# Kernel optimization log

Measured on AMD Instinct MI355X. Metric: run time of the kernel, lower is better.

Reference implementation:

```python
import jax, jax.numpy as jnp
import numpy as np

IN_DIM = 3
OUT_DIM = 3
HSI_DIM = 31
MIN_BAND = 400.0
MAX_BAND = 700.0
N_BAND = 31  # == HSI_DIM so the indexed write fills every column
BN_EPS = 1e-5


def setup_inputs() -> dict:
    key = jax.random.key(0)
    ks = jax.random.split(key, 8)
    B, H, W = 16, 256, 256
    x = jax.random.uniform(ks[0], (B, H, W, IN_DIM), jnp.float32)
    x_hsi = jax.random.uniform(ks[1], (B, H, W, HSI_DIM), jnp.float32)
    conv_w = jax.random.normal(ks[2], (64, IN_DIM, 3, 3), jnp.float32) * 0.1
    conv_b = jax.random.normal(ks[3], (64,), jnp.float32) * 0.1
    bn_w = 1.0 + jax.random.normal(ks[4], (64,), jnp.float32) * 0.1
    bn_b = jax.random.normal(ks[5], (64,), jnp.float32) * 0.1
    fc_w = jax.random.normal(ks[6], (OUT_DIM + 2, 64), jnp.float32) * 0.1
    fc_b = jax.random.normal(ks[7], (OUT_DIM + 2,), jnp.float32) * 0.1
    return {"x": x, "x_hsi": x_hsi, "conv_w": conv_w, "conv_b": conv_b,
            "bn_w": bn_w, "bn_b": bn_b, "fc_w": fc_w, "fc_b": fc_b}


def _voltage_net(x, conv_w, conv_b, bn_w, bn_b, fc_w, fc_b):
    # x: (B, H, W, 3) channels-last -> NCHW
    xp = jnp.transpose(x, (0, 3, 1, 2))
    y = jax.lax.conv_general_dilated(
        xp, conv_w, window_strides=(1, 1), padding='SAME',
        dimension_numbers=('NCHW', 'OIHW', 'NCHW')) + conv_b[None, :, None, None]
    # BatchNorm2d (training-mode batch statistics, biased variance)
    mu = y.mean(axis=(0, 2, 3))
    var = y.var(axis=(0, 2, 3))
    y = (y - mu[None, :, None, None]) * jax.lax.rsqrt(var + BN_EPS)[None, :, None, None]
    y = y * bn_w[None, :, None, None] + bn_b[None, :, None, None]
    y = jax.nn.relu(y)
    feat = y.mean(axis=(2, 3))                      # AdaptiveAvgPool2d(1) -> (B, 64)
    raw = feat @ fc_w.T + fc_b                      # (B, out_dim + 2)
    mn = raw.min(axis=1, keepdims=True)
    mx = raw.max(axis=1, keepdims=True)
    norm = (raw - mn) / (mx - mn + 1e-8)
    mid = jnp.sort(norm, axis=1)[:, 1:-1]           # drop smallest & largest
    return mid * 10.0                               # (B, out_dim) voltages


def reference(x, x_hsi, conv_w, conv_b, bn_w, bn_b, fc_w, fc_b):
    voltages = _voltage_net(x, conv_w, conv_b, bn_w, bn_b, fc_w, fc_b)  # (B, C)
    # Vectorized Lyot SRF (replaces per-batch python loop); nBand == hsi_dim
    n = jnp.arange(N_BAND, dtype=jnp.float32)
    band = MIN_BAND + (MAX_BAND - MIN_BAND) * n / N_BAND                # (A,)
    cos_part = jnp.cos(2.0 * jnp.pi * (-0.01) / voltages)               # (B, C)
    srf = (0.5 - 0.5 * cos_part)[:, :, None] / (band[None, None, :] * 1e-6)  # (B, C, A)
    # contract hyperspectral bands: (B,C,A) x (B,H,W,A) -> (B,H,W,C)
    return jnp.einsum('bca,bpqa->bpqc', srf, x_hsi)
```

## Files before the change

kernel.cpp:

```cpp
#include <hip/hip_runtime.h>
#include <hip/hip_bf16.h>
#include <math.h>

#define BB 16
#define HH 256
#define WW 256

#define OFF_CHSUM 0
#define OFF_CHSQ  64
#define OFF_FEAT  256
#define OFF_Z     2048

#define SM_PAN   0
#define SM_W     21728
#define SM_B     28640
#define SM_RED   28896
#define SM_G     31744
#define SM_BYTES 32000

typedef __attribute__((ext_vector_type(8))) short bf16x8;
typedef __attribute__((ext_vector_type(4))) float f32x4;

union BFu { __hip_bfloat16 h; short s; };
union ABu { bf16x8 v; unsigned u[4]; };

__device__ __forceinline__ unsigned packsplit(float v) {
    BFu hi; hi.h = __float2bfloat16(v);
    float rs = v - __bfloat162float(hi.h);
    BFu lo; lo.h = __float2bfloat16(rs);
    return (unsigned)(unsigned short)hi.s | ((unsigned)(unsigned short)lo.s << 16);
}

__global__ void k_init(float* __restrict__ ws) {
    int i = blockIdx.x * 256 + threadIdx.x;
    if (i < 1280) ws[i] = 0.f;
}

template <int MODE>
__global__ __launch_bounds__(256) void k_convz(const float* __restrict__ x,
                                               const float* __restrict__ xh,
                                               const float* __restrict__ cw,
                                               const float* __restrict__ cb,
                                               const float* __restrict__ bnw,
                                               const float* __restrict__ bnb,
                                               float* __restrict__ ws) {
    __shared__ __align__(16) char smem[SM_BYTES];
    const int t = threadIdx.x;
    const int b = blockIdx.y;

    if (blockIdx.x >= 64) {
        float* s_x = (float*)smem;
        float* s_g = (float*)(smem + SM_G);
        const int zx = blockIdx.x - 64;
        if (t < 31) {
            const float band = 400.f + (300.f * (float)t) / 31.f;
            s_g[t] = 1.f / (band * 1e-6f);
        }
#pragma unroll 1
        for (int c = 0; c < 8; ++c) {
            const size_t pxbase = (size_t)b * 65536 + zx * 2048 + c * 256;
            const float4* xg = (const float4*)(xh + pxbase * 31);
            float4* sx4 = (float4*)s_x;
#pragma unroll
            for (int i = 0; i < 8; ++i) {
                int idx = t + (i << 8);
                if (idx < 1984) sx4[idx] = xg[idx];
            }
            __syncthreads();
            float z = 0.f;
            const float* px = s_x + t * 31;
#pragma unroll
            for (int a = 0; a < 31; ++a) z = fmaf(px[a], s_g[a], z);
            ws[OFF_Z + pxbase + t] = z;
            __syncthreads();
        }
        return;
    }

    unsigned* pan32 = (unsigned*)smem;
    float* s_w = (float*)(smem + SM_W);
    float* s_b = (float*)(smem + SM_B);
    float (*red)[4][16][2] = (float (*)[4][16][2])(smem + SM_RED);

    const int lane = t & 63;
    const int wv   = t >> 6;
    const int r0   = blockIdx.x * 4;
    const int mrow = lane & 15;
    const int s    = lane >> 4;
    const bool s3  = (s == 3);
    const float* __restrict__ xb = x + (size_t)b * (HH * WW * 3);

    for (int i = t; i < 1728; i += 256) s_w[i] = cw[i];
    if (t < 64) s_b[t] = cb[t];

    for (int e = t; e < 6 * 774; e += 256) {
        const int l = e / 774, j = e - l * 774;
        const int gr = r0 - 1 + l, gcf = j - 3;
        const bool ok = ((unsigned)gr < 256u) && ((unsigned)gcf < 768u);
        int off = gr * 768 + gcf;
        off = ok ? off : 0;
        float v = xb[off];
        v = ok ? v : 0.f;
        pan32[l * 776 + j] = packsplit(v);
    }
    for (int j = t; j < 776; j += 256) pan32[6 * 776 + j] = 0x3F80u;

    float av[4], bvv[4];
#pragma unroll
    for (int n = 0; n < 4; ++n) {
        const int ch = n * 16 + mrow;
        if (MODE == 1) {
            const float invN = 1.f / 1048576.f;
            const float mu = ws[OFF_CHSUM + ch] * invN;
            const float vr = ws[OFF_CHSQ + ch] * invN - mu * mu;
            const float rs = rsqrtf(vr + 1e-5f);
            av[n]  = rs * bnw[ch];
            bvv[n] = bnb[ch] - mu * av[n];
        } else { av[n] = 1.f; bvv[n] = 0.f; }
    }

    int off8[8];
#pragma unroll
    for (int e = 0; e < 8; ++e) {
        if (!s3)        off8[e] = (wv + s) * 776 + e;
        else if (e < 3) off8[e] = (wv + e) * 776 + 8;
        else            off8[e] = 6 * 776 + e;
    }
    const int mrow3 = mrow * 3;

    __syncthreads();

    bf16x8 bh[4], bl[4];
#pragma unroll
    for (int n = 0; n < 4; ++n) {
        const int ch = n * 16 + mrow;
#pragma unroll
        for (int e = 0; e < 8; ++e) {
            float w = 0.f;
            if (!s3) {
                w = s_w[ch * 27 + (e % 3) * 9 + s * 3 + (e / 3)];
            } else if (e < 3) {
                w = s_w[ch * 27 + 18 + e * 3 + 2];
            } else if (e == 3) {
                w = s_b[ch];
            }
            if (MODE == 1) {
                w *= av[n];
                if (s3 && e == 3) w += bvv[n];
            }
            BFu hi; hi.h = __float2bfloat16(w);
            const float rs2 = w - __bfloat162float(hi.h);
            BFu lo; lo.h = __float2bfloat16(rs2);
            bh[n][e] = hi.s;
            bl[n][e] = lo.s;
        }
    }

    float a0[4] = {0.f, 0.f, 0.f, 0.f};
    float a1[4] = {0.f, 0.f, 0.f, 0.f};

#define GATHER(W, CS)                                                   \
    {                                                                   \
        const int c3 = (CS) * 48 + mrow3;                               \
        W[0] = pan32[off8[0] + c3]; W[1] = pan32[off8[1] + c3];         \
        W[2] = pan32[off8[2] + c3]; W[3] = pan32[off8[3] + c3];         \
        W[4] = pan32[off8[4] + c3]; W[5] = pan32[off8[5] + c3];         \
        W[6] = pan32[off8[6] + c3]; W[7] = pan32[off8[7] + c3];         \
    }
#define COMPUTE(W)                                                      \
    {                                                                   \
        ABu ua, ul;                                                     \
        ua.u[0] = __builtin_amdgcn_perm(W[1], W[0], 0x05040100u);       \
        ua.u[1] = __builtin_amdgcn_perm(W[3], W[2], 0x05040100u);       \
        ua.u[2] = __builtin_amdgcn_perm(W[5], W[4], 0x05040100u);       \
        ua.u[3] = __builtin_amdgcn_perm(W[7], W[6], 0x05040100u);       \
        ul.u[0] = __builtin_amdgcn_perm(W[1], W[0], 0x07060302u);       \
        ul.u[1] = __builtin_amdgcn_perm(W[3], W[2], 0x07060302u);       \
        ul.u[2] = __builtin_amdgcn_perm(W[5], W[4], 0x07060302u);       \
        ul.u[3] = __builtin_amdgcn_perm(W[7], W[6], 0x07060302u);       \
        const bf16x8 ah = ua.v, al = ul.v;                              \
        __builtin_amdgcn_s_setprio(1);                                  \
        _Pragma("unroll")                                               \
        for (int n = 0; n < 4; ++n) {                                   \
            f32x4 acc = {0.f, 0.f, 0.f, 0.f};                           \
            acc = __builtin_amdgcn_mfma_f32_16x16x32_bf16(ah, bl[n], acc, 0, 0, 0); \
            acc = __builtin_amdgcn_mfma_f32_16x16x32_bf16(al, bh[n], acc, 0, 0, 0); \
            acc = __builtin_amdgcn_mfma_f32_16x16x32_bf16(ah, bh[n], acc, 0, 0, 0); \
            _Pragma("unroll")                                           \
            for (int i = 0; i < 4; ++i) {                               \
                const float y = acc[i];                                 \
                if (MODE == 0) { a0[n] += y; a1[n] = fmaf(y, y, a1[n]); } \
                else { a0[n] += fmaxf(y, 0.f); }                        \
            }                                                           \
        }                                                               \
        __builtin_amdgcn_s_setprio(0);                                  \
    }

    {
        unsigned Wa[8], Wb[8];
        GATHER(Wa, 0)
        GATHER(Wb, 1)  COMPUTE(Wa)
        GATHER(Wa, 2)  COMPUTE(Wb)
        GATHER(Wb, 3)  COMPUTE(Wa)
        GATHER(Wa, 4)  COMPUTE(Wb)
        GATHER(Wb, 5)  COMPUTE(Wa)
        GATHER(Wa, 6)  COMPUTE(Wb)
        GATHER(Wb, 7)  COMPUTE(Wa)
        GATHER(Wa, 8)  COMPUTE(Wb)
        GATHER(Wb, 9)  COMPUTE(Wa)
        GATHER(Wa, 10) COMPUTE(Wb)
        GATHER(Wb, 11) COMPUTE(Wa)
        GATHER(Wa, 12) COMPUTE(Wb)
        GATHER(Wb, 13) COMPUTE(Wa)
        GATHER(Wa, 14) COMPUTE(Wb)
        GATHER(Wb, 15) COMPUTE(Wa)
        COMPUTE(Wb)
    }
#undef GATHER
#undef COMPUTE

#pragma unroll
    for (int n = 0; n < 4; ++n) {
        a0[n] += __shfl_xor(a0[n], 16);
        a0[n] += __shfl_xor(a0[n], 32);
        if (MODE == 0) {
            a1[n] += __shfl_xor(a1[n], 16);
            a1[n] += __shfl_xor(a1[n], 32);
        }
    }
    if (lane < 16) {
#pragma unroll
        for (int n = 0; n < 4; ++n) {
            red[wv][n][lane][0] = a0[n];
            red[wv][n][lane][1] = (MODE == 0) ? a1[n] : 0.f;
        }
    }
    __syncthreads();
    if (t < 64) {
        const int n = t >> 4, m = t & 15;
        const float S = red[0][n][m][0] + red[1][n][m][0] + red[2][n][m][0] + red[3][n][m][0];
        if (MODE == 0) {
            const float Q = red[0][n][m][1] + red[1][n][m][1] + red[2][n][m][1] + red[3][n][m][1];
            atomicAdd(&ws[OFF_CHSUM + t], S);
            atomicAdd(&ws[OFF_CHSQ + t], Q);
        } else {
            atomicAdd(&ws[OFF_FEAT + b * 64 + t], S);
        }
    }
}

__global__ __launch_bounds__(256) void k_final3(const float* __restrict__ fcw,
                                                const float* __restrict__ fcb,
                                                const float* __restrict__ ws,
                                                float* __restrict__ out) {
    __shared__ float s_z[1024];
    __shared__ float s_raw[5];
    __shared__ float sp[3];
    const int t = threadIdx.x;
    const int blk = blockIdx.x;
    const int b = blk >> 6;
    const size_t pix0 = (size_t)blk << 10;

    if (t < 5) {
        const float inv = 1.f / 65536.f;
        float a = fcb[t];
        for (int c = 0; c < 64; ++c)
            a = fmaf(fcw[t * 64 + c], ws[OFF_FEAT + b * 64 + c] * inv, a);
        s_raw[t] = a;
    }
    ((float4*)s_z)[t] = ((const float4*)(ws + OFF_Z + pix0))[t];
    __syncthreads();
    if (t == 0) {
        float raw[5];
#pragma unroll
        for (int j = 0; j < 5; ++j) raw[j] = s_raw[j];
#define CS(i, j)                              \
        {                                     \
            float lo = fminf(raw[i], raw[j]); \
            float hi = fmaxf(raw[i], raw[j]); \
            raw[i] = lo;                      \
            raw[j] = hi;                      \
        }
        CS(0, 1) CS(3, 4) CS(2, 4) CS(2, 3) CS(0, 3) CS(0, 2) CS(1, 4) CS(1, 3) CS(1, 2)
#undef CS
        const float mn = raw[0], mx = raw[4];
        const float sc = 10.f / (mx - mn + 1e-8f);
#pragma unroll
        for (int c2 = 0; c2 < 3; ++c2) {
            const float v = (raw[1 + c2] - mn) * sc;
            const float sh = sinf(0.031415926535897934f / v);
            sp[c2] = sh * sh;
        }
    }
    __syncthreads();
    float4* ob = (float4*)(out + pix0 * 3);
#pragma unroll
    for (int k = 0; k < 3; ++k) {
        const int j = t + (k << 8);
        const int f = 4 * j;
        float4 v;
        v.x = sp[(f + 0) % 3] * s_z[(f + 0) / 3];
        v.y = sp[(f + 1) % 3] * s_z[(f + 1) / 3];
        v.z = sp[(f + 2) % 3] * s_z[(f + 2) / 3];
        v.w = sp[(f + 3) % 3] * s_z[(f + 3) / 3];
        ob[j] = v;
    }
}

extern "C" void kernel_launch(void* const* d_in, const int* in_sizes, int n_in,
                              void* d_out, int out_size, void* d_ws, size_t ws_size,
                              hipStream_t stream) {
    const float* x    = (const float*)d_in[0];
    const float* xhsi = (const float*)d_in[1];
    const float* cw   = (const float*)d_in[2];
    const float* cb   = (const float*)d_in[3];
    const float* bnw  = (const float*)d_in[4];
    const float* bnb  = (const float*)d_in[5];
    const float* fcw  = (const float*)d_in[6];
    const float* fcb  = (const float*)d_in[7];
    float* out = (float*)d_out;
    float* ws  = (float*)d_ws;

    hipLaunchKernelGGL(k_init, dim3(5), dim3(256), 0, stream, ws);
    hipLaunchKernelGGL((k_convz<0>), dim3(96, 16), dim3(256), 0, stream,
                       x, xhsi, cw, cb, bnw, bnb, ws);
    hipLaunchKernelGGL((k_convz<1>), dim3(64, 16), dim3(256), 0, stream,
                       x, xhsi, cw, cb, bnw, bnb, ws);
    hipLaunchKernelGGL(k_final3, dim3(1024), dim3(256), 0, stream, fcw, fcb, ws, out);
}
```

Before: 81.58 us.

## Compute BN statistics from the patch Gram matrix instead of a full conv pass

The first conv pass, which only computed per-channel sums and squares for BatchNorm, is replaced by a kernel that accumulates a 28x28 Gram matrix of the im2col patches (27 taps plus a bias row) using split-bf16 MFMAs. A single-block kernel then derives each channel's mean and second moment as w^T G w. This removes the 64-channel conv work from the stats pass, since the Gram matrix does not depend on channel count. In exchange it adds a tiny serial kernel launch, more atomics per block (1792 per block), and possible precision change in the variance.

New measurement: 89.75 us. 1.1x slower.

```diff
diff --git a/kernel.cpp b/kernel.cpp
--- a/kernel.cpp
+++ b/kernel.cpp
@@ -10,6 +10,7 @@
 #define OFF_CHSQ  64
 #define OFF_FEAT  256
 #define OFF_Z     2048
+#define OFF_G     1050624
 
 #define SM_PAN   0
 #define SM_W     21728
@@ -34,16 +35,12 @@
 __global__ void k_init(float* __restrict__ ws) {
     int i = blockIdx.x * 256 + threadIdx.x;
     if (i < 1280) ws[i] = 0.f;
-}
-
-template <int MODE>
-__global__ __launch_bounds__(256) void k_convz(const float* __restrict__ x,
-                                               const float* __restrict__ xh,
-                                               const float* __restrict__ cw,
-                                               const float* __restrict__ cb,
-                                               const float* __restrict__ bnw,
-                                               const float* __restrict__ bnb,
-                                               float* __restrict__ ws) {
+    if (i < 1792) ws[OFF_G + i] = 0.f;
+}
+
+__global__ __launch_bounds__(256) void k_gram(const float* __restrict__ x,
+                                              const float* __restrict__ xh,
+                                              float* __restrict__ ws) {
     __shared__ __align__(16) char smem[SM_BYTES];
     const int t = threadIdx.x;
     const int b = blockIdx.y;
@@ -78,20 +75,13 @@
     }
 
     unsigned* pan32 = (unsigned*)smem;
-    float* s_w = (float*)(smem + SM_W);
-    float* s_b = (float*)(smem + SM_B);
-    float (*red)[4][16][2] = (float (*)[4][16][2])(smem + SM_RED);
-
+    float* red = (float*)(smem + SM_W);
     const int lane = t & 63;
     const int wv   = t >> 6;
     const int r0   = blockIdx.x * 4;
     const int mrow = lane & 15;
-    const int s    = lane >> 4;
-    const bool s3  = (s == 3);
+    const int ksl  = lane >> 4;
     const float* __restrict__ xb = x + (size_t)b * (HH * WW * 3);
-
-    for (int i = t; i < 1728; i += 256) s_w[i] = cw[i];
-    if (t < 64) s_b[t] = cb[t];
 
     for (int e = t; e < 6 * 774; e += 256) {
         const int l = e / 774, j = e - l * 774;
@@ -105,18 +95,198 @@
     }
     for (int j = t; j < 776; j += 256) pan32[6 * 776 + j] = 0x3F80u;
 
+    const int kh0 = mrow / 9, jj0 = mrow - kh0 * 9;
+    const int base0 = (wv + kh0) * 776 + jj0;
+    const int t1 = 16 + mrow;
+    const int base1 = (t1 < 27) ? ((wv + t1 / 9) * 776 + (t1 % 9)) : (6 * 776);
+    const int coltrm = 3 * (ksl * 8);
+
+    __syncthreads();
+
+    f32x4 hh00 = {0.f,0.f,0.f,0.f}, hh01 = {0.f,0.f,0.f,0.f}, hh11 = {0.f,0.f,0.f,0.f};
+    f32x4 hl00 = {0.f,0.f,0.f,0.f}, hl01 = {0.f,0.f,0.f,0.f};
+    f32x4 hl10 = {0.f,0.f,0.f,0.f}, hl11 = {0.f,0.f,0.f,0.f};
+
+#define GG(W0, W1, J)                                                    \
+    {                                                                    \
+        const int cofs = coltrm + 96 * (J);                              \
+        W0[0] = pan32[base0 + cofs +  0]; W0[1] = pan32[base0 + cofs +  3]; \
+        W0[2] = pan32[base0 + cofs +  6]; W0[3] = pan32[base0 + cofs +  9]; \
+        W0[4] = pan32[base0 + cofs + 12]; W0[5] = pan32[base0 + cofs + 15]; \
+        W0[6] = pan32[base0 + cofs + 18]; W0[7] = pan32[base0 + cofs + 21]; \
+        W1[0] = pan32[base1 + cofs +  0]; W1[1] = pan32[base1 + cofs +  3]; \
+        W1[2] = pan32[base1 + cofs +  6]; W1[3] = pan32[base1 + cofs +  9]; \
+        W1[4] = pan32[base1 + cofs + 12]; W1[5] = pan32[base1 + cofs + 15]; \
+        W1[6] = pan32[base1 + cofs + 18]; W1[7] = pan32[base1 + cofs + 21]; \
+    }
+#define CG(W0, W1)                                                       \
+    {                                                                    \
+        ABu h0, l0, h1, l1;                                              \
+        h0.u[0] = __builtin_amdgcn_perm(W0[1], W0[0], 0x05040100u);      \
+        h0.u[1] = __builtin_amdgcn_perm(W0[3], W0[2], 0x05040100u);      \
+        h0.u[2] = __builtin_amdgcn_perm(W0[5], W0[4], 0x05040100u);      \
+        h0.u[3] = __builtin_amdgcn_perm(W0[7], W0[6], 0x05040100u);      \
+        l0.u[0] = __builtin_amdgcn_perm(W0[1], W0[0], 0x07060302u);      \
+        l0.u[1] = __builtin_amdgcn_perm(W0[3], W0[2], 0x07060302u);      \
+        l0.u[2] = __builtin_amdgcn_perm(W0[5], W0[4], 0x07060302u);      \
+        l0.u[3] = __builtin_amdgcn_perm(W0[7], W0[6], 0x07060302u);      \
+        h1.u[0] = __builtin_amdgcn_perm(W1[1], W1[0], 0x05040100u);      \
+        h1.u[1] = __builtin_amdgcn_perm(W1[3], W1[2], 0x05040100u);      \
+        h1.u[2] = __builtin_amdgcn_perm(W1[5], W1[4], 0x05040100u);      \
+        h1.u[3] = __builtin_amdgcn_perm(W1[7], W1[6], 0x05040100u);      \
+        l1.u[0] = __builtin_amdgcn_perm(W1[1], W1[0], 0x07060302u);      \
+        l1.u[1] = __builtin_amdgcn_perm(W1[3], W1[2], 0x07060302u);      \
+        l1.u[2] = __builtin_amdgcn_perm(W1[5], W1[4], 0x07060302u);      \
+        l1.u[3] = __builtin_amdgcn_perm(W1[7], W1[6], 0x07060302u);      \
+        hh00 = __builtin_amdgcn_mfma_f32_16x16x32_bf16(h0.v, h0.v, hh00, 0, 0, 0); \
+        hh01 = __builtin_amdgcn_mfma_f32_16x16x32_bf16(h0.v, h1.v, hh01, 0, 0, 0); \
+        hh11 = __builtin_amdgcn_mfma_f32_16x16x32_bf16(h1.v, h1.v, hh11, 0, 0, 0); \
+        hl00 = __builtin_amdgcn_mfma_f32_16x16x32_bf16(h0.v, l0.v, hl00, 0, 0, 0); \
+        hl01 = __builtin_amdgcn_mfma_f32_16x16x32_bf16(h0.v, l1.v, hl01, 0, 0, 0); \
+        hl10 = __builtin_amdgcn_mfma_f32_16x16x32_bf16(h1.v, l0.v, hl10, 0, 0, 0); \
+        hl11 = __builtin_amdgcn_mfma_f32_16x16x32_bf16(h1.v, l1.v, hl11, 0, 0, 0); \
+    }
+
+    {
+        unsigned Wa0[8], Wa1[8], Wb0[8], Wb1[8];
+        GG(Wa0, Wa1, 0)
+        GG(Wb0, Wb1, 1)  CG(Wa0, Wa1)
+        GG(Wa0, Wa1, 2)  CG(Wb0, Wb1)
+        GG(Wb0, Wb1, 3)  CG(Wa0, Wa1)
+        GG(Wa0, Wa1, 4)  CG(Wb0, Wb1)
+        GG(Wb0, Wb1, 5)  CG(Wa0, Wa1)
+        GG(Wa0, Wa1, 6)  CG(Wb0, Wb1)
+        GG(Wb0, Wb1, 7)  CG(Wa0, Wa1)
+        CG(Wb0, Wb1)
+    }
+#undef GG
+#undef CG
+
+    const int row0 = ksl * 4;
+#define STW(TI, A, OP)                                                   \
+    red[(TI) * 256 + (row0 + 0) * 16 + mrow] OP A[0];                    \
+    red[(TI) * 256 + (row0 + 1) * 16 + mrow] OP A[1];                    \
+    red[(TI) * 256 + (row0 + 2) * 16 + mrow] OP A[2];                    \
+    red[(TI) * 256 + (row0 + 3) * 16 + mrow] OP A[3];
+    if (wv == 0) { STW(0,hh00,=)  STW(1,hh01,=)  STW(2,hh11,=)
+                   STW(3,hl00,=)  STW(4,hl01,=)  STW(5,hl10,=)  STW(6,hl11,=) }
+    __syncthreads();
+    if (wv == 1) { STW(0,hh00,+=) STW(1,hh01,+=) STW(2,hh11,+=)
+                   STW(3,hl00,+=) STW(4,hl01,+=) STW(5,hl10,+=) STW(6,hl11,+=) }
+    __syncthreads();
+    if (wv == 2) { STW(0,hh00,+=) STW(1,hh01,+=) STW(2,hh11,+=)
+                   STW(3,hl00,+=) STW(4,hl01,+=) STW(5,hl10,+=) STW(6,hl11,+=) }
+    __syncthreads();
+    if (wv == 3) { STW(0,hh00,+=) STW(1,hh01,+=) STW(2,hh11,+=)
+                   STW(3,hl00,+=) STW(4,hl01,+=) STW(5,hl10,+=) STW(6,hl11,+=) }
+    __syncthreads();
+#undef STW
+    for (int i = t; i < 1792; i += 256) atomicAdd(&ws[OFF_G + i], red[i]);
+}
+
+__device__ __forceinline__ float HHf(const float* G, int t, int u) {
+    if (t < 16 && u < 16) return G[t * 16 + u];
+    if (t < 16)           return G[256 + t * 16 + (u - 16)];
+    if (u < 16)           return G[256 + u * 16 + (t - 16)];
+    return G[512 + (t - 16) * 16 + (u - 16)];
+}
+__device__ __forceinline__ float HLf(const float* G, int t, int u) {
+    if (t < 16 && u < 16) return G[768 + t * 16 + u];
+    if (t < 16)           return G[1024 + t * 16 + (u - 16)];
+    if (u < 16)           return G[1280 + (t - 16) * 16 + u];
+    return G[1536 + (t - 16) * 16 + (u - 16)];
+}
+
+__global__ __launch_bounds__(256) void k_stats2(const float* __restrict__ cw,
+                                                const float* __restrict__ cb,
+                                                float* __restrict__ ws) {
+    __shared__ float Gs[28 * 28];
+    __shared__ float Sp[4][64], Qp[4][64];
+    const int t = threadIdx.x;
+    const float* Gg = ws + OFF_G;
+    for (int e = t; e < 784; e += 256) {
+        const int i = e / 28, j = e - i * 28;
+        Gs[e] = HHf(Gg, i, j) + HLf(Gg, i, j) + HLf(Gg, j, i);
+    }
+    __syncthreads();
+    const int ch = t & 63, qq = t >> 6;
+    float wt[28];
+#pragma unroll
+    for (int k = 0; k < 27; ++k) {
+        const int kh = k / 9, jj = k - kh * 9, kw = jj / 3, ci = jj - kw * 3;
+        wt[k] = cw[ch * 27 + ci * 9 + kh * 3 + kw];
+    }
+    wt[27] = cb[ch];
+    float S = 0.f, Q = 0.f;
+    for (int i = qq * 7; i < qq * 7 + 7; ++i) {
+        const float wi = wt[i];
+        S = fmaf(wi, Gs[i * 28 + 27], S);
+        float qrow = 0.f;
+#pragma unroll
+        for (int j = 0; j < 28; ++j) qrow = fmaf(wt[j], Gs[i * 28 + j], qrow);
+        Q = fmaf(wi, qrow, Q);
+    }
+    Sp[qq][ch] = S;
+    Qp[qq][ch] = Q;
+    __syncthreads();
+    if (t < 64) {
+        ws[OFF_CHSUM + t] = Sp[0][t] + Sp[1][t] + Sp[2][t] + Sp[3][t];
+        ws[OFF_CHSQ + t]  = Qp[0][t] + Qp[1][t] + Qp[2][t] + Qp[3][t];
+    }
+}
+
+template <int MODE>
+__global__ __launch_bounds__(256) void k_convz(const float* __restrict__ x,
+                                               const float* __restrict__ xh,
+                                               const float* __restrict__ cw,
+                                               const float* __restrict__ cb,
+                                               const float* __restrict__ bnw,
+                                               const float* __restrict__ bnb,
+                                               float* __restrict__ ws) {
+    __shared__ __align__(16) char smem[SM_BYTES];
+    const int t = threadIdx.x;
+    const int b = blockIdx.y;
+
+    if (blockIdx.x >= 64) return;
+
+    unsigned* pan32 = (unsigned*)smem;
+    float* s_w = (float*)(smem + SM_W);
+    float* s_b = (float*)(smem + SM_B);
+    float (*red)[4][16][2] = (float (*)[4][16][2])(smem + SM_RED);
+
+    const int lane = t & 63;
+    const int wv   = t >> 6;
+    const int r0   = blockIdx.x * 4;
+    const int mrow = lane & 15;
+    const int s    = lane >> 4;
+    const bool s3  = (s == 3);
+    const float* __restrict__ xb = x + (size_t)b * (HH * WW * 3);
+
+    for (int i = t; i < 1728; i += 256) s_w[i] = cw[i];
+    if (t < 64) s_b[t] = cb[t];
+
+    for (int e = t; e < 6 * 774; e += 256) {
+        const int l = e / 774, j = e - l * 774;
+        const int gr = r0 - 1 + l, gcf = j - 3;
+        const bool ok = ((unsigned)gr < 256u) && ((unsigned)gcf < 768u);
+        int off = gr * 768 + gcf;
+        off = ok ? off : 0;
+        float v = xb[off];
+        v = ok ? v : 0.f;
+        pan32[l * 776 + j] = packsplit(v);
+    }
+    for (int j = t; j < 776; j += 256) pan32[6 * 776 + j] = 0x3F80u;
+
     float av[4], bvv[4];
 #pragma unroll
     for (int n = 0; n < 4; ++n) {
         const int ch = n * 16 + mrow;
-        if (MODE == 1) {
-            const float invN = 1.f / 1048576.f;
-            const float mu = ws[OFF_CHSUM + ch] * invN;
-            const float vr = ws[OFF_CHSQ + ch] * invN - mu * mu;
-            const float rs = rsqrtf(vr + 1e-5f);
-            av[n]  = rs * bnw[ch];
-            bvv[n] = bnb[ch] - mu * av[n];
-        } else { av[n] = 1.f; bvv[n] = 0.f; }
+        const float invN = 1.f / 1048576.f;
+        const float mu = ws[OFF_CHSUM + ch] * invN;
+        const float vr = ws[OFF_CHSQ + ch] * invN - mu * mu;
+        const float rs = rsqrtf(vr + 1e-5f);
+        av[n]  = rs * bnw[ch];
+        bvv[n] = bnb[ch] - mu * av[n];
     }
 
     int off8[8];
@@ -137,17 +307,11 @@
 #pragma unroll
         for (int e = 0; e < 8; ++e) {
             float w = 0.f;
-            if (!s3) {
-                w = s_w[ch * 27 + (e % 3) * 9 + s * 3 + (e / 3)];
-            } else if (e < 3) {
-                w = s_w[ch * 27 + 18 + e * 3 + 2];
-            } else if (e == 3) {
-                w = s_b[ch];
-            }
-            if (MODE == 1) {
-                w *= av[n];
-                if (s3 && e == 3) w += bvv[n];
-            }
+            if (!s3)        w = s_w[ch * 27 + (e % 3) * 9 + s * 3 + (e / 3)];
+            else if (e < 3) w = s_w[ch * 27 + 18 + e * 3 + 2];
+            else if (e == 3) w = s_b[ch];
+            w *= av[n];
+            if (s3 && e == 3) w += bvv[n];
             BFu hi; hi.h = __float2bfloat16(w);
             const float rs2 = w - __bfloat162float(hi.h);
             BFu lo; lo.h = __float2bfloat16(rs2);
@@ -157,7 +321,6 @@
     }
 
     float a0[4] = {0.f, 0.f, 0.f, 0.f};
-    float a1[4] = {0.f, 0.f, 0.f, 0.f};
 
 #define GATHER(W, CS)                                                   \
     {                                                                   \
@@ -187,11 +350,7 @@
             acc = __builtin_amdgcn_mfma_f32_16x16x32_bf16(al, bh[n], acc, 0, 0, 0); \
             acc = __builtin_amdgcn_mfma_f32_16x16x32_bf16(ah, bh[n], acc, 0, 0, 0); \
             _Pragma("unroll")                                           \
-            for (int i = 0; i < 4; ++i) {                               \
-                const float y = acc[i];                                 \
-                if (MODE == 0) { a0[n] += y; a1[n] = fmaf(y, y, a1[n]); } \
-                else { a0[n] += fmaxf(y, 0.f); }                        \
-            }                                                           \
+            for (int i = 0; i < 4; ++i) a0[n] += fmaxf(acc[i], 0.f);    \
         }                                                               \
         __builtin_amdgcn_s_setprio(0);                                  \
     }
@@ -223,29 +382,16 @@
     for (int n = 0; n < 4; ++n) {
         a0[n] += __shfl_xor(a0[n], 16);
         a0[n] += __shfl_xor(a0[n], 32);
-        if (MODE == 0) {
-            a1[n] += __shfl_xor(a1[n], 16);
-            a1[n] += __shfl_xor(a1[n], 32);
-        }
     }
     if (lane < 16) {
 #pragma unroll
-        for (int n = 0; n < 4; ++n) {
-            red[wv][n][lane][0] = a0[n];
-            red[wv][n][lane][1] = (MODE == 0) ? a1[n] : 0.f;
-        }
+        for (int n = 0; n < 4; ++n) red[wv][n][lane][0] = a0[n];
     }
     __syncthreads();
     if (t < 64) {
         const int n = t >> 4, m = t & 15;
         const float S = red[0][n][m][0] + red[1][n][m][0] + red[2][n][m][0] + red[3][n][m][0];
-        if (MODE == 0) {
-            const float Q = red[0][n][m][1] + red[1][n][m][1] + red[2][n][m][1] + red[3][n][m][1];
-            atomicAdd(&ws[OFF_CHSUM + t], S);
-            atomicAdd(&ws[OFF_CHSQ + t], Q);
-        } else {
-            atomicAdd(&ws[OFF_FEAT + b * 64 + t], S);
-        }
+        atomicAdd(&ws[OFF_FEAT + b * 64 + t], S);
     }
 }
 
@@ -321,9 +467,9 @@
     float* out = (float*)d_out;
     float* ws  = (float*)d_ws;
 
-    hipLaunchKernelGGL(k_init, dim3(5), dim3(256), 0, stream, ws);
-    hipLaunchKernelGGL((k_convz<0>), dim3(96, 16), dim3(256), 0, stream,
-                       x, xhsi, cw, cb, bnw, bnb, ws);
+    hipLaunchKernelGGL(k_init, dim3(7), dim3(256), 0, stream, ws);
+    hipLaunchKernelGGL(k_gram, dim3(96, 16), dim3(256), 0, stream, x, xhsi, ws);
+    hipLaunchKernelGGL(k_stats2, dim3(1), dim3(256), 0, stream, cw, cb, ws);
     hipLaunchKernelGGL((k_convz<1>), dim3(64, 16), dim3(256), 0, stream,
                        x, xhsi, cw, cb, bnw, bnb, ws);
     hipLaunchKernelGGL(k_final3, dim3(1024), dim3(256), 0, stream, fcw, fcb, ws, out);
```

## Materialize conv output as bf16 in workspace instead of recomputing conv

Applied to the files above, without the earlier changes.

Adds a fast path in which the first pass writes the conv outputs to workspace as bf16 alongside the BN statistics. A second kernel then reads them back to apply BN, ReLU and pooling, instead of recomputing the MFMA convolution. This trades a second conv pass for about 128MB of writes and 128MB of reads. It also rounds y to bf16 before the BN affine, which may hurt accuracy. The path is taken only when the workspace is large enough.

Result: slower. 106.7 us (+30.8%).

```diff
diff --git a/kernel.cpp b/kernel.cpp
--- a/kernel.cpp
+++ b/kernel.cpp
@@ -10,6 +10,9 @@
 #define OFF_CHSQ  64
 #define OFF_FEAT  256
 #define OFF_Z     2048
+#define OFF_Y     1050624
+#define Y_DWORDS  33554432ull
+#define WS_FAST_BYTES (((size_t)OFF_Y + Y_DWORDS) * 4)
 
 #define SM_PAN   0
 #define SM_W     21728
@@ -31,9 +34,264 @@
     return (unsigned)(unsigned short)hi.s | ((unsigned)(unsigned short)lo.s << 16);
 }
 
+__device__ __forceinline__ unsigned packbf2(float a, float b) {
+    BFu x; x.h = __float2bfloat16(a);
+    BFu y; y.h = __float2bfloat16(b);
+    return (unsigned)(unsigned short)x.s | ((unsigned)(unsigned short)y.s << 16);
+}
+
 __global__ void k_init(float* __restrict__ ws) {
     int i = blockIdx.x * 256 + threadIdx.x;
     if (i < 1280) ws[i] = 0.f;
+}
+
+__global__ __launch_bounds__(256) void k_convy(const float* __restrict__ x,
+                                               const float* __restrict__ xh,
+                                               const float* __restrict__ cw,
+                                               const float* __restrict__ cb,
+                                               float* __restrict__ ws) {
+    __shared__ __align__(16) char smem[SM_BYTES];
+    const int t = threadIdx.x;
+    const int b = blockIdx.y;
+
+    if (blockIdx.x >= 64) {
+        float* s_x = (float*)smem;
+        float* s_g = (float*)(smem + SM_G);
+        const int zx = blockIdx.x - 64;
+        if (t < 31) {
+            const float band = 400.f + (300.f * (float)t) / 31.f;
+            s_g[t] = 1.f / (band * 1e-6f);
+        }
+#pragma unroll 1
+        for (int c = 0; c < 8; ++c) {
+            const size_t pxbase = (size_t)b * 65536 + zx * 2048 + c * 256;
+            const float4* xg = (const float4*)(xh + pxbase * 31);
+            float4* sx4 = (float4*)s_x;
+#pragma unroll
+            for (int i = 0; i < 8; ++i) {
+                int idx = t + (i << 8);
+                if (idx < 1984) sx4[idx] = xg[idx];
+            }
+            __syncthreads();
+            float z = 0.f;
+            const float* px = s_x + t * 31;
+#pragma unroll
+            for (int a = 0; a < 31; ++a) z = fmaf(px[a], s_g[a], z);
+            ws[OFF_Z + pxbase + t] = z;
+            __syncthreads();
+        }
+        return;
+    }
+
+    unsigned* pan32 = (unsigned*)smem;
+    float* s_w = (float*)(smem + SM_W);
+    float* s_b = (float*)(smem + SM_B);
+    float (*red)[4][16][2] = (float (*)[4][16][2])(smem + SM_RED);
+
+    const int lane = t & 63;
+    const int wv   = t >> 6;
+    const int r0   = blockIdx.x * 4;
+    const int mrow = lane & 15;
+    const int s    = lane >> 4;
+    const bool s3  = (s == 3);
+    const float* __restrict__ xb = x + (size_t)b * (HH * WW * 3);
+
+    for (int i = t; i < 1728; i += 256) s_w[i] = cw[i];
+    if (t < 64) s_b[t] = cb[t];
+
+    for (int e = t; e < 6 * 774; e += 256) {
+        const int l = e / 774, j = e - l * 774;
+        const int gr = r0 - 1 + l, gcf = j - 3;
+        const bool ok = ((unsigned)gr < 256u) && ((unsigned)gcf < 768u);
+        int off = gr * 768 + gcf;
+        off = ok ? off : 0;
+        float v = xb[off];
+        v = ok ? v : 0.f;
+        pan32[l * 776 + j] = packsplit(v);
+    }
+    for (int j = t; j < 776; j += 256) pan32[6 * 776 + j] = 0x3F80u;
+
+    int off8[8];
+#pragma unroll
+    for (int e = 0; e < 8; ++e) {
+        if (!s3)        off8[e] = (wv + s) * 776 + e;
+        else if (e < 3) off8[e] = (wv + e) * 776 + 8;
+        else            off8[e] = 6 * 776 + e;
+    }
+    const int mrow3 = mrow * 3;
+
+    __syncthreads();
+
+    bf16x8 bh[4], bl[4];
+#pragma unroll
+    for (int n = 0; n < 4; ++n) {
+        const int ch = n * 16 + mrow;
+#pragma unroll
+        for (int e = 0; e < 8; ++e) {
+            float w = 0.f;
+            if (!s3)        w = s_w[ch * 27 + (e % 3) * 9 + s * 3 + (e / 3)];
+            else if (e < 3) w = s_w[ch * 27 + 18 + e * 3 + 2];
+            else if (e == 3) w = s_b[ch];
+            BFu hi; hi.h = __float2bfloat16(w);
+            const float rs2 = w - __bfloat162float(hi.h);
+            BFu lo; lo.h = __float2bfloat16(rs2);
+            bh[n][e] = hi.s;
+            bl[n][e] = lo.s;
+        }
+    }
+
+    float a0[4] = {0.f, 0.f, 0.f, 0.f};
+    float a1[4] = {0.f, 0.f, 0.f, 0.f};
+    unsigned* const Ybase = (unsigned*)(ws + OFF_Y);
+    const size_t gtbase = (size_t)b * 4096 + (size_t)(r0 + wv) * 16;
+
+#define GATHER(W, CS)                                                   \
+    {                                                                   \
+        const int c3 = (CS) * 48 + mrow3;                               \
+        W[0] = pan32[off8[0] + c3]; W[1] = pan32[off8[1] + c3];         \
+        W[2] = pan32[off8[2] + c3]; W[3] = pan32[off8[3] + c3];         \
+        W[4] = pan32[off8[4] + c3]; W[5] = pan32[off8[5] + c3];         \
+        W[6] = pan32[off8[6] + c3]; W[7] = pan32[off8[7] + c3];         \
+    }
+#define COMPUTEY(W, CS)                                                 \
+    {                                                                   \
+        ABu ua, ul;                                                     \
+        ua.u[0] = __builtin_amdgcn_perm(W[1], W[0], 0x05040100u);       \
+        ua.u[1] = __builtin_amdgcn_perm(W[3], W[2], 0x05040100u);       \
+        ua.u[2] = __builtin_amdgcn_perm(W[5], W[4], 0x05040100u);       \
+        ua.u[3] = __builtin_amdgcn_perm(W[7], W[6], 0x05040100u);       \
+        ul.u[0] = __builtin_amdgcn_perm(W[1], W[0], 0x07060302u);       \
+        ul.u[1] = __builtin_amdgcn_perm(W[3], W[2], 0x07060302u);       \
+        ul.u[2] = __builtin_amdgcn_perm(W[5], W[4], 0x07060302u);       \
+        ul.u[3] = __builtin_amdgcn_perm(W[7], W[6], 0x07060302u);       \
+        const bf16x8 ah = ua.v, al = ul.v;                              \
+        unsigned pk[8];                                                 \
+        __builtin_amdgcn_s_setprio(1);                                  \
+        _Pragma("unroll")                                               \
+        for (int n = 0; n < 4; ++n) {                                   \
+            f32x4 acc = {0.f, 0.f, 0.f, 0.f};                           \
+            acc = __builtin_amdgcn_mfma_f32_16x16x32_bf16(ah, bl[n], acc, 0, 0, 0); \
+            acc = __builtin_amdgcn_mfma_f32_16x16x32_bf16(al, bh[n], acc, 0, 0, 0); \
+            acc = __builtin_amdgcn_mfma_f32_16x16x32_bf16(ah, bh[n], acc, 0, 0, 0); \
+            pk[n * 2 + 0] = packbf2(acc[0], acc[1]);                    \
+            pk[n * 2 + 1] = packbf2(acc[2], acc[3]);                    \
+            _Pragma("unroll")                                           \
+            for (int i = 0; i < 4; ++i) {                               \
+                const float y = acc[i];                                 \
+                a0[n] += y; a1[n] = fmaf(y, y, a1[n]);                  \
+            }                                                           \
+        }                                                               \
+        __builtin_amdgcn_s_setprio(0);                                  \
+        {                                                               \
+            unsigned* yp = Ybase + ((gtbase + (CS)) << 9) + (lane << 3);\
+            *(uint4*)yp       = make_uint4(pk[0], pk[1], pk[2], pk[3]); \
+            *((uint4*)yp + 1) = make_uint4(pk[4], pk[5], pk[6], pk[7]); \
+        }                                                               \
+    }
+
+    {
+        unsigned Wa[8], Wb[8];
+        GATHER(Wa, 0)
+        GATHER(Wb, 1)  COMPUTEY(Wa, 0)
+        GATHER(Wa, 2)  COMPUTEY(Wb, 1)
+        GATHER(Wb, 3)  COMPUTEY(Wa, 2)
+        GATHER(Wa, 4)  COMPUTEY(Wb, 3)
+        GATHER(Wb, 5)  COMPUTEY(Wa, 4)
+        GATHER(Wa, 6)  COMPUTEY(Wb, 5)
+        GATHER(Wb, 7)  COMPUTEY(Wa, 6)
+        GATHER(Wa, 8)  COMPUTEY(Wb, 7)
+        GATHER(Wb, 9)  COMPUTEY(Wa, 8)
+        GATHER(Wa, 10) COMPUTEY(Wb, 9)
+        GATHER(Wb, 11) COMPUTEY(Wa, 10)
+        GATHER(Wa, 12) COMPUTEY(Wb, 11)
+        GATHER(Wb, 13) COMPUTEY(Wa, 12)
+        GATHER(Wa, 14) COMPUTEY(Wb, 13)
+        GATHER(Wb, 15) COMPUTEY(Wa, 14)
+        COMPUTEY(Wb, 15)
+    }
+#undef GATHER
+#undef COMPUTEY
+
+#pragma unroll
+    for (int n = 0; n < 4; ++n) {
+        a0[n] += __shfl_xor(a0[n], 16);
+        a0[n] += __shfl_xor(a0[n], 32);
+        a1[n] += __shfl_xor(a1[n], 16);
+        a1[n] += __shfl_xor(a1[n], 32);
+    }
+    if (lane < 16) {
+#pragma unroll
+        for (int n = 0; n < 4; ++n) {
+            red[wv][n][lane][0] = a0[n];
+            red[wv][n][lane][1] = a1[n];
+        }
+    }
+    __syncthreads();
+    if (t < 64) {
+        const int n = t >> 4, m = t & 15;
+        const float S = red[0][n][m][0] + red[1][n][m][0] + red[2][n][m][0] + red[3][n][m][0];
+        const float Q = red[0][n][m][1] + red[1][n][m][1] + red[2][n][m][1] + red[3][n][m][1];
+        atomicAdd(&ws[OFF_CHSUM + t], S);
+        atomicAdd(&ws[OFF_CHSQ + t], Q);
+    }
+}
+
+__global__ __launch_bounds__(256) void k_bnpool(const float* __restrict__ bnw,
+                                                const float* __restrict__ bnb,
+                                                float* __restrict__ ws) {
+    __shared__ float red[4][4][16];
+    const int t = threadIdx.x;
+    const int b = blockIdx.y;
+    const int lane = t & 63;
+    const int wv = t >> 6;
+    const int mrow = lane & 15;
+
+    float A[4], Bc[4];
+#pragma unroll
+    for (int n = 0; n < 4; ++n) {
+        const int ch = n * 16 + mrow;
+        const float invN = 1.f / 1048576.f;
+        const float mu = ws[OFF_CHSUM + ch] * invN;
+        const float vr = ws[OFF_CHSQ + ch] * invN - mu * mu;
+        const float rs = rsqrtf(vr + 1e-5f);
+        A[n]  = rs * bnw[ch];
+        Bc[n] = bnb[ch] - mu * A[n];
+    }
+
+    const unsigned* const Y = (const unsigned*)(ws + OFF_Y);
+    float a0[4] = {0.f, 0.f, 0.f, 0.f};
+#pragma unroll 1
+    for (int it = 0; it < 16; ++it) {
+        const size_t gt = (size_t)b * 4096 + blockIdx.x * 64 + it * 4 + wv;
+        const uint4* p = (const uint4*)(Y + (gt << 9) + (lane << 3));
+        const uint4 d0 = p[0];
+        const uint4 d1 = p[1];
+#define UNP(dw, n)                                                    \
+        {                                                             \
+            const float y0 = __uint_as_float((dw) << 16);             \
+            const float y1 = __uint_as_float((dw) & 0xFFFF0000u);     \
+            a0[n] += fmaxf(fmaf(y0, A[n], Bc[n]), 0.f);               \
+            a0[n] += fmaxf(fmaf(y1, A[n], Bc[n]), 0.f);               \
+        }
+        UNP(d0.x, 0) UNP(d0.y, 0) UNP(d0.z, 1) UNP(d0.w, 1)
+        UNP(d1.x, 2) UNP(d1.y, 2) UNP(d1.z, 3) UNP(d1.w, 3)
+#undef UNP
+    }
+#pragma unroll
+    for (int n = 0; n < 4; ++n) {
+        a0[n] += __shfl_xor(a0[n], 16);
+        a0[n] += __shfl_xor(a0[n], 32);
+    }
+    if (lane < 16) {
+#pragma unroll
+        for (int n = 0; n < 4; ++n) red[wv][n][mrow] = a0[n];
+    }
+    __syncthreads();
+    if (t < 64) {
+        const int n = t >> 4, m = t & 15;
+        atomicAdd(&ws[OFF_FEAT + b * 64 + t],
+                  red[0][n][m] + red[1][n][m] + red[2][n][m] + red[3][n][m]);
+    }
 }
 
 template <int MODE>
@@ -137,13 +395,9 @@
 #pragma unroll
         for (int e = 0; e < 8; ++e) {
             float w = 0.f;
-            if (!s3) {
-                w = s_w[ch * 27 + (e % 3) * 9 + s * 3 + (e / 3)];
-            } else if (e < 3) {
-                w = s_w[ch * 27 + 18 + e * 3 + 2];
-            } else if (e == 3) {
-                w = s_b[ch];
-            }
+            if (!s3)        w = s_w[ch * 27 + (e % 3) * 9 + s * 3 + (e / 3)];
+            else if (e < 3) w = s_w[ch * 27 + 18 + e * 3 + 2];
+            else if (e == 3) w = s_b[ch];
             if (MODE == 1) {
                 w *= av[n];
                 if (s3 && e == 3) w += bvv[n];
@@ -322,9 +576,15 @@
     float* ws  = (float*)d_ws;
 
     hipLaunchKernelGGL(k_init, dim3(5), dim3(256), 0, stream, ws);
-    hipLaunchKernelGGL((k_convz<0>), dim3(96, 16), dim3(256), 0, stream,
-                       x, xhsi, cw, cb, bnw, bnb, ws);
-    hipLaunchKernelGGL((k_convz<1>), dim3(64, 16), dim3(256), 0, stream,
-                       x, xhsi, cw, cb, bnw, bnb, ws);
+    if (ws_size >= WS_FAST_BYTES) {
+        hipLaunchKernelGGL(k_convy, dim3(96, 16), dim3(256), 0, stream,
+                           x, xhsi, cw, cb, ws);
+        hipLaunchKernelGGL(k_bnpool, dim3(64, 16), dim3(256), 0, stream, bnw, bnb, ws);
+    } else {
+        hipLaunchKernelGGL((k_convz<0>), dim3(96, 16), dim3(256), 0, stream,
+                           x, xhsi, cw, cb, bnw, bnb, ws);
+        hipLaunchKernelGGL((k_convz<1>), dim3(64, 16), dim3(256), 0, stream,
+                           x, xhsi, cw, cb, bnw, bnb, ws);
+    }
     hipLaunchKernelGGL(k_final3, dim3(1024), dim3(256), 0, stream, fcw, fcb, ws, out);
 }
```
